# Kernel optimization log

Measured on AMD Instinct MI355X. Metric: run time of the kernel, lower is better.

## Reference

```python
import jax, jax.numpy as jnp
import numpy as np

NUM_HEADS = 12


def _attend(q, k, v, scale):
    # q: [B,H,Q,D], k/v: [B,H,K,D]
    attn = jnp.einsum('bhqd,bhkd->bhqk', q, k) * scale
    attn = jax.nn.softmax(attn, axis=-1)
    return jnp.einsum('bhqk,bhkd->bhqd', attn, v)


def setup_inputs() -> dict:
    key = jax.random.key(0)
    k1, k2, k3 = jax.random.split(key, 3)
    B, N, C = 32, 1009, 768
    x = jax.random.normal(k1, (B, N, C), dtype=jnp.float32)
    W_qkv = jax.random.normal(k2, (C, 3 * C), dtype=jnp.float32) * (C ** -0.5)
    b_qkv = jnp.zeros((3 * C,), dtype=jnp.float32)
    W_proj = jax.random.normal(k3, (C, C), dtype=jnp.float32) * (C ** -0.5)
    b_proj = jnp.zeros((C,), dtype=jnp.float32)
    return {"x": x, "W_qkv": W_qkv, "b_qkv": b_qkv, "W_proj": W_proj,
            "b_proj": b_proj, "query_len": 1, "lens_z": 432}


def reference(x, W_qkv, b_qkv, W_proj, b_proj, query_len, lens_z):
    B, N, C = x.shape
    H = NUM_HEADS
    D = C // H
    scale = D ** -0.5
    lens_x = N - query_len - lens_z

    qkv = (x @ W_qkv + b_qkv).reshape(B, N, 3, H, D)
    qkv = jnp.transpose(qkv, (2, 0, 3, 1, 4))  # [3,B,H,N,D]
    q, k, v = qkv[0], qkv[1], qkv[2]

    sl_p = slice(0, query_len)
    sl_t = slice(query_len, query_len + lens_z)
    sl_s = slice(query_len + lens_z, N)

    # prompt: local self-attention
    x_prompt = _attend(q[:, :, sl_p], k[:, :, sl_p], v[:, :, sl_p], scale)
    # template: local self-attention
    x_template = _attend(q[:, :, sl_t], k[:, :, sl_t], v[:, :, sl_t], scale)
    # search: global attention over all tokens
    x_search = _attend(q[:, :, sl_s], k, v, scale)

    def merge(y, L):
        return jnp.transpose(y, (0, 2, 1, 3)).reshape(B, L, C)

    out = jnp.concatenate([merge(x_prompt, query_len),
                           merge(x_template, lens_z),
                           merge(x_search, lens_x)], axis=1)
    return out @ W_proj + b_proj
```

## Files before the change

kernel.cpp:

```cpp
#include <hip/hip_runtime.h>

#define B_ 32
#define N_ 1009
#define C_ 768
#define H_ 12
#define D_ 64
#define M_ (B_*N_)
#define MT_ 253
#define MPAD_ (MT_*128)
#define NKV_ 1024

typedef __attribute__((ext_vector_type(4))) float f32x4;
typedef __attribute__((ext_vector_type(8))) short s16x8;

__device__ __forceinline__ unsigned short f2bf(float f) {
  union { float f; unsigned u; } x; x.f = f;
  unsigned r = x.u + 0x7fffu + ((x.u >> 16) & 1u);
  return (unsigned short)(r >> 16);
}

__device__ __forceinline__ f32x4 mfma16(s16x8 a, s16x8 b, f32x4 c) {
  return __builtin_amdgcn_mfma_f32_16x16x32_bf16(a, b, c, 0, 0, 0);
}

__device__ __forceinline__ void async16(const void* g, void* l) {
  __builtin_amdgcn_global_load_lds((const __attribute__((address_space(1))) void*)g,
                                   (__attribute__((address_space(3))) void*)l, 16, 0, 0);
}

__device__ __forceinline__ float exp2_fast(float x) {
  float r; asm("v_exp_f32 %0, %1" : "=v"(r) : "v"(x)); return r;
}

__device__ __forceinline__ unsigned cvt_pk_bf16(float lo, float hi) {
  unsigned r; asm("v_cvt_pk_bf16_f32 %0, %1, %2" : "=v"(r) : "v"(lo), "v"(hi)); return r;
}

template<int NWG>
__device__ __forceinline__ int xcd_swz(int bid) {
  constexpr int q = NWG >> 3, r = NWG & 7;
  const int x = bid & 7, l = bid >> 3;
  return (x < r ? x * (q + 1) : r * (q + 1) + (x - r) * q) + l;
}

__global__ void convert_x(const float* __restrict__ x, unsigned short* __restrict__ xb) {
  const long e = ((long)blockIdx.x * 256 + threadIdx.x) * 8;
  const long row = e / 768;
  s16x8 v;
  if (row < M_) {
#pragma unroll
    for (int j = 0; j < 8; ++j) v[j] = (short)f2bf(x[e + j]);
  } else {
    v = (s16x8){0,0,0,0,0,0,0,0};
  }
  *(s16x8*)&xb[e] = v;
}

__global__ void transpose_convert(const float* __restrict__ in, unsigned short* __restrict__ out,
                                  int R, int Ccols) {
  __shared__ float tile[64][65];
  const int tc = blockIdx.x * 64, tr = blockIdx.y * 64;
#pragma unroll
  for (int i = 0; i < 16; ++i) {
    const int e = i * 256 + threadIdx.x;
    const int r = e >> 6, c = e & 63;
    tile[r][c] = in[(long)(tr + r) * Ccols + tc + c];
  }
  __syncthreads();
#pragma unroll
  for (int i = 0; i < 16; ++i) {
    const int e = i * 256 + threadIdx.x;
    const int c = e >> 6, r = e & 63;
    out[(long)(tc + c) * R + tr + r] = f2bf(tile[r][c]);
  }
}

__global__ void zero_pad(unsigned short* __restrict__ kb, unsigned short* __restrict__ vt) {
  const int t = blockIdx.x * 256 + threadIdx.x;
  if (t >= 368640) return;
  const int d = t & 63;
  const int r = t >> 6;
  const int bh = r / 15, tok = 1009 + (r - bh * 15);
  kb[(((long)bh << 10) + tok) * 64 + d] = 0;
  const int c = t % 15, row = t / 15;
  vt[((long)row << 10) + 1009 + c] = 0;
}

template<int MODE>
__global__ __launch_bounds__(256, 4)
void gemm_bt(const unsigned short* __restrict__ A,
             const unsigned short* __restrict__ Bt,
             const float* __restrict__ bias,
             unsigned short* __restrict__ qo,
             unsigned short* __restrict__ ko,
             unsigned short* __restrict__ vo,
             float* __restrict__ fo) {
  __shared__ __align__(16) unsigned short smem[17408];
  const int tid = threadIdx.x;
  const int lane = tid & 63;
  const int wv = tid >> 6;
  constexpr int NBN = (MODE == 0) ? 18 : 6;
  const int swzid = xcd_swz<MT_ * NBN>(blockIdx.x);
  const int bm = swzid / NBN;
  const int bn = swzid - bm * NBN;
  const int row0 = bm * 128;
  const int col0 = bn * 128;
  const int wr = (wv >> 1) * 64;
  const int wc = (wv & 1) * 64;

  auto stage = [&](int bufsel, int kt) {
#pragma unroll
    for (int c = 0; c < 2; ++c) {
      const int lds_off = c * 4096 + wv * 1024;
      const int gg = c * 256 + wv * 64 + lane;
      const int row = gg >> 2;
      const int ck = ((gg & 3) ^ ((row >> 1) & 3)) << 3;
      async16(A + (long)(row0 + row) * 768 + kt + ck, (char*)smem + bufsel * 8192 + lds_off);
      async16(Bt + (long)(col0 + row) * 768 + kt + ck, (char*)smem + 16384 + bufsel * 8192 + lds_off);
    }
  };

  f32x4 acc[4][4] = {};
  stage(0, 0);
  for (int it = 0; it < 24; ++it) {
    const int buf = it & 1;
    if (it + 1 < 24) {
      stage(buf ^ 1, (it + 1) * 32);
      asm volatile("s_waitcnt vmcnt(4)" ::: "memory");
    } else {
      asm volatile("s_waitcnt vmcnt(0)" ::: "memory");
    }
    __builtin_amdgcn_s_barrier();

    const unsigned short* Asb = smem + buf * 4096;
    const unsigned short* Bsb = smem + 8192 + buf * 4096;
    s16x8 af[4], bfr[4];
#pragma unroll
    for (int m = 0; m < 4; ++m) {
      const int rA = wr + m * 16 + (lane & 15);
      af[m] = *(const s16x8*)&Asb[rA * 32 + (((lane >> 4) ^ ((rA >> 1) & 3)) << 3)];
    }
#pragma unroll
    for (int n = 0; n < 4; ++n) {
      const int rB = wc + n * 16 + (lane & 15);
      bfr[n] = *(const s16x8*)&Bsb[rB * 32 + (((lane >> 4) ^ ((rB >> 1) & 3)) << 3)];
    }
    __builtin_amdgcn_s_setprio(1);
#pragma unroll
    for (int m = 0; m < 4; ++m)
#pragma unroll
      for (int n = 0; n < 4; ++n)
        acc[m][n] = mfma16(af[m], bfr[n], acc[m][n]);
    __builtin_amdgcn_s_setprio(0);

    asm volatile("s_waitcnt lgkmcnt(0)" ::: "memory");
    __builtin_amdgcn_s_barrier();
  }

  if (MODE == 0 && col0 < 1536) {
    const int qsel = col0 < 768;
#pragma unroll
    for (int m = 0; m < 4; ++m)
#pragma unroll
      for (int j = 0; j < 4; ++j)
#pragma unroll
        for (int n = 0; n < 4; ++n) {
          const int tk = wr + m * 16 + (lane >> 4) * 4 + j;
          const int cl = wc + n * 16 + (lane & 15);
          float val = acc[m][n][j] + bias[col0 + cl];
          if (qsel) val *= 0.18033688011112042f;
          smem[tk * 136 + cl] = f2bf(val);
        }
    __syncthreads();
    unsigned short* const dst = qsel ? qo : ko;
    const int colb = col0 - (qsel ? 0 : 768);
#pragma unroll
    for (int it = 0; it < 8; ++it) {
      const int g = it * 256 + tid;
      const int tk = g >> 4;
      const int ch = (g & 15) * 8;
      const int grow = row0 + tk;
      if (grow < M_) {
        const s16x8 vv = *(const s16x8*)&smem[tk * 136 + ch];
        const int b = grow / N_;
        const int ntok = grow - b * N_;
        const int rem = colb + ch;
        const int h = rem >> 6, d = rem & 63;
        *(s16x8*)&dst[(((((long)b * H_ + h) << 10) + ntok) << 6) + d] = vv;
      }
    }
    return;
  }

  if (MODE == 0) {
#pragma unroll
    for (int m = 0; m < 4; ++m)
#pragma unroll
      for (int j = 0; j < 4; ++j)
#pragma unroll
        for (int n = 0; n < 4; ++n) {
          const int dl = wc + n * 16 + (lane & 15);
          const int tk = wr + m * 16 + (lane >> 4) * 4 + j;
          smem[dl * 136 + tk] = f2bf(acc[m][n][j] + bias[col0 + dl]);
        }
    __syncthreads();
    const int h0 = (col0 - 1536) >> 6;
    const int b0 = row0 / N_;
    const int split = (b0 + 1) * N_ - row0;
#pragma unroll
    for (int it = 0; it < 8; ++it) {
      const int g = it * 256 + tid;
      const int dl = g >> 4;
      const int t8 = (g & 15) * 8;
      const s16x8 vv = *(const s16x8*)&smem[dl * 136 + t8];
      const int hh = h0 + (dl >> 6), dd = dl & 63;
#pragma unroll
      for (int jj = 0; jj < 8; ++jj) {
        const int tkb = t8 + jj;
        const int grow = row0 + tkb;
        if (grow < M_) {
          const int bb = (tkb < split) ? b0 : b0 + 1;
          const int ntok = grow - bb * N_;
          vo[(((((long)bb * H_ + hh) << 6) + dd) << 10) + ntok] = (unsigned short)vv[jj];
        }
      }
    }
    return;
  }

#pragma unroll
  for (int m = 0; m < 4; ++m) {
#pragma unroll
    for (int j = 0; j < 4; ++j) {
      const int grow = row0 + wr + m * 16 + (lane >> 4) * 4 + j;
      if (grow < M_) {
#pragma unroll
        for (int n = 0; n < 4; ++n) {
          const int col = col0 + wc + n * 16 + (lane & 15);
          fo[(long)grow * 768 + col] = acc[m][n][j] + bias[col];
        }
      }
    }
  }
}

__global__ void misc_copy(const unsigned short* __restrict__ vt, unsigned short* __restrict__ og) {
  const int t = blockIdx.x * 256 + threadIdx.x;
  if (t >= B_ * H_ * D_) return;
  const int d = t & 63;
  const int bh = t >> 6;
  const int b = bh / H_, h = bh - b * H_;
  og[((long)b * N_) * 768 + h * 64 + d] = vt[(((long)bh << 6) + d) << 10];
}

__global__ __launch_bounds__(256, 4)
void attn_kernel(const unsigned short* __restrict__ qg,
                 const unsigned short* __restrict__ kg,
                 const unsigned short* __restrict__ vtg,
                 unsigned short* __restrict__ og) {
  __shared__ __align__(16) unsigned short Ks[2][64 * 64];
  __shared__ __align__(16) unsigned short Vts[2][64 * 64];
  __shared__ __align__(16) unsigned short Ps[64 * 64];

  const int bid = blockIdx.x;
  const int swz = (bid & 7) * 768 + (bid >> 3);
  const int tile = swz & 15;
  const int bh = swz >> 4;
  const int b = bh / H_;
  const int h = bh - b * H_;
  int qbase, qend, kstart, ktiles, kend;
  if (tile < 7) { qbase = 1 + 64 * tile;       qend = 433;  kstart = 1; ktiles = 7;  kend = 433; }
  else          { qbase = 433 + 64 * (tile-7); qend = 1009; kstart = 0; ktiles = 16; kend = 1009; }
  const long base  = (long)bh << 10;
  const long vbase = (long)bh << 6;
  const int tid = threadIdx.x, lane = tid & 63, wv = tid >> 6;
  const int q15 = lane & 15, q7 = lane & 7, g = lane >> 4;

  s16x8 qa[2];
  {
    const unsigned short* qp = qg + (base + qbase + wv * 16 + q15) * 64;
    qa[0] = *(const s16x8*)(qp + g * 8);
    qa[1] = *(const s16x8*)(qp + 32 + g * 8);
  }
  asm volatile("s_waitcnt vmcnt(0)" ::: "memory");

  f32x4 o[4] = {};
  float mrow = -1e30f, lrow = 0.f;

  auto stage = [&](int bufsel, int kb0) {
#pragma unroll
    for (int it = 0; it < 2; ++it) {
      const int ldsoff = (it * 256 + wv * 64) * 16;
      const int gr = it * 256 + wv * 64 + lane;
      const int rl = gr >> 3;
      const int cs = (gr & 7) ^ (rl & 7);
      async16(kg + ((base + kb0 + rl) << 6) + cs * 8, (char*)&Ks[bufsel][0] + ldsoff);
      async16(vtg + ((vbase + rl) << 10) + kb0 + cs * 8, (char*)&Vts[bufsel][0] + ldsoff);
    }
  };

  const int prow = wv * 16 + q15;

  stage(0, kstart);
  for (int kt = 0; kt < ktiles; ++kt) {
    const int buf = kt & 1;
    const int kbase0 = kstart + 64 * kt;
    if (kt + 1 < ktiles) {
      stage(buf ^ 1, kbase0 + 64);
      asm volatile("s_waitcnt vmcnt(4)" ::: "memory");
    } else {
      asm volatile("s_waitcnt vmcnt(0)" ::: "memory");
    }
    __builtin_amdgcn_s_barrier();

    f32x4 s4[4];
    __builtin_amdgcn_s_setprio(1);
#pragma unroll
    for (int n = 0; n < 4; ++n) {
      const int krow = n * 16 + q15;
      const int r7 = krow & 7;
      f32x4 a = {};
      a = mfma16(*(const s16x8*)&Ks[buf][krow * 64 + ((g ^ r7) << 3)],       qa[0], a);
      a = mfma16(*(const s16x8*)&Ks[buf][krow * 64 + (((4 + g) ^ r7) << 3)], qa[1], a);
      s4[n] = a;
    }
    __builtin_amdgcn_s_setprio(0);

    if (kbase0 + 64 > kend) {
#pragma unroll
      for (int n = 0; n < 4; ++n)
#pragma unroll
        for (int j = 0; j < 4; ++j)
          if (kbase0 + n * 16 + g * 4 + j >= kend) s4[n][j] = -1e30f;
    }

    float rmax = fmaxf(
        fmaxf(fmaxf(fmaxf(s4[0][0], s4[0][1]), fmaxf(s4[0][2], s4[0][3])),
              fmaxf(fmaxf(s4[1][0], s4[1][1]), fmaxf(s4[1][2], s4[1][3]))),
        fmaxf(fmaxf(fmaxf(s4[2][0], s4[2][1]), fmaxf(s4[2][2], s4[2][3])),
              fmaxf(fmaxf(s4[3][0], s4[3][1]), fmaxf(s4[3][2], s4[3][3]))));
    rmax = fmaxf(rmax, __shfl_xor(rmax, 16));
    rmax = fmaxf(rmax, __shfl_xor(rmax, 32));

    const float mnew = fmaxf(mrow, rmax);
    const float corr = exp2_fast(mrow - mnew);
    mrow = mnew;
#pragma unroll
    for (int f = 0; f < 4; ++f)
#pragma unroll
      for (int j = 0; j < 4; ++j) o[f][j] *= corr;

    float psum = 0.f;
#pragma unroll
    for (int n = 0; n < 4; ++n) {
#pragma unroll
      for (int j = 0; j < 4; ++j) {
        s4[n][j] = exp2_fast(s4[n][j] - mnew);
        psum += s4[n][j];
      }
      uint2 pw;
      pw.x = cvt_pk_bf16(s4[n][0], s4[n][1]);
      pw.y = cvt_pk_bf16(s4[n][2], s4[n][3]);
      *(uint2*)((char*)Ps + prow * 128 + (((n * 2 + (g >> 1)) ^ q7) << 4) + (g & 1) * 8) = pw;
    }
    psum += __shfl_xor(psum, 16);
    psum += __shfl_xor(psum, 32);
    lrow = lrow * corr + psum;

    s16x8 pa[2];
#pragma unroll
    for (int kf = 0; kf < 2; ++kf)
      pa[kf] = *(const s16x8*)((char*)Ps + prow * 128 + (((kf * 4 + g) ^ q7) << 4));
    __builtin_amdgcn_s_setprio(1);
#pragma unroll
    for (int f = 0; f < 4; ++f) {
      const int vrow = f * 16 + q15;
      const int v7 = vrow & 7;
#pragma unroll
      for (int kf = 0; kf < 2; ++kf) {
        const s16x8 vb = *(const s16x8*)&Vts[buf][vrow * 64 + (((kf * 4 + g) ^ v7) << 3)];
        o[f] = mfma16(vb, pa[kf], o[f]);
      }
    }
    __builtin_amdgcn_s_setprio(0);

    asm volatile("s_waitcnt lgkmcnt(0)" ::: "memory");
    __builtin_amdgcn_s_barrier();
  }

  const int qrow = qbase + wv * 16 + q15;
  if (qrow < qend) {
    const float inv = 1.0f / lrow;
    unsigned short* op = og + ((long)b * N_ + qrow) * 768 + h * 64 + g * 4;
#pragma unroll
    for (int f = 0; f < 4; ++f) {
      uint2 ow;
      ow.x = cvt_pk_bf16(o[f][0] * inv, o[f][1] * inv);
      ow.y = cvt_pk_bf16(o[f][2] * inv, o[f][3] * inv);
      *(uint2*)(op + f * 16) = ow;
    }
  }
}

extern "C" void kernel_launch(void* const* d_in, const int* in_sizes, int n_in,
                              void* d_out, int out_size, void* d_ws, size_t ws_size,
                              hipStream_t stream) {
  const float* x      = (const float*)d_in[0];
  const float* W_qkv  = (const float*)d_in[1];
  const float* b_qkv  = (const float*)d_in[2];
  const float* W_proj = (const float*)d_in[3];
  const float* b_proj = (const float*)d_in[4];
  float* out = (float*)d_out;

  unsigned short* ws = (unsigned short*)d_ws;
  unsigned short* wqkvT  = ws;
  unsigned short* wprojT = wqkvT + (long)2304 * 768;
  unsigned short* qb = wprojT + (long)768 * 768;
  const long kvsz = (long)B_ * H_ * NKV_ * D_;
  unsigned short* kb = qb + kvsz;
  unsigned short* vb = kb + kvsz;
  unsigned short* xb = vb + kvsz;
  unsigned short* attnout = xb;

  zero_pad<<<1440, 256, 0, stream>>>(kb, vb);
  convert_x<<<12144, 256, 0, stream>>>(x, xb);
  transpose_convert<<<dim3(2304 / 64, 768 / 64), 256, 0, stream>>>(W_qkv, wqkvT, 768, 2304);
  transpose_convert<<<dim3(768 / 64, 768 / 64), 256, 0, stream>>>(W_proj, wprojT, 768, 768);
  gemm_bt<0><<<MT_ * 18, 256, 0, stream>>>(xb, wqkvT, b_qkv, qb, kb, vb, nullptr);
  misc_copy<<<96, 256, 0, stream>>>(vb, attnout);
  attn_kernel<<<B_ * H_ * 16, 256, 0, stream>>>(qb, kb, vb, attnout);
  gemm_bt<1><<<MT_ * 6, 256, 0, stream>>>(attnout, wprojT, b_proj, nullptr, nullptr, nullptr, out);
}
```

Before: 405.2 us.

## Use 32x32x16 MFMA in GEMM and skip softmax rescale when max barely moves

The QKV and projection GEMM inner loop switches from 16x16x32 to 32x32x16 bf16 MFMA tiles. This changes fragment loads, the LDS swizzle pattern and the epilogue index mapping, with the goal of fewer LDS reads and instructions per FLOP. Separately, the attention kernel uses lazy rescaling: the running max, and the rescale of the output and row sum, are only updated when some row's new max exceeds the old one by more than 8 in log2 units. This saves the correction multiplies but lets unnormalised exponentials grow up to 2^8, which carries some risk of bf16 precision loss in P.

```diff
diff --git a/kernel.cpp b/kernel.cpp
--- a/kernel.cpp
+++ b/kernel.cpp
@@ -11,6 +11,7 @@
 #define NKV_ 1024
 
 typedef __attribute__((ext_vector_type(4))) float f32x4;
+typedef __attribute__((ext_vector_type(16))) float f32x16;
 typedef __attribute__((ext_vector_type(8))) short s16x8;
 
 __device__ __forceinline__ unsigned short f2bf(float f) {
@@ -21,6 +22,10 @@
 
 __device__ __forceinline__ f32x4 mfma16(s16x8 a, s16x8 b, f32x4 c) {
   return __builtin_amdgcn_mfma_f32_16x16x32_bf16(a, b, c, 0, 0, 0);
+}
+
+__device__ __forceinline__ f32x16 mfma32(s16x8 a, s16x8 b, f32x16 c) {
+  return __builtin_amdgcn_mfma_f32_32x32x16_bf16(a, b, c, 0, 0, 0);
 }
 
 __device__ __forceinline__ void async16(const void* g, void* l) {
@@ -107,6 +112,7 @@
   const int col0 = bn * 128;
   const int wr = (wv >> 1) * 64;
   const int wc = (wv & 1) * 64;
+  const int l31 = lane & 31, hi = lane >> 5;
 
   auto stage = [&](int bufsel, int kt) {
 #pragma unroll
@@ -114,13 +120,13 @@
       const int lds_off = c * 4096 + wv * 1024;
       const int gg = c * 256 + wv * 64 + lane;
       const int row = gg >> 2;
-      const int ck = ((gg & 3) ^ ((row >> 1) & 3)) << 3;
+      const int ck = ((gg & 3) ^ (((row >> 1) ^ (row >> 3)) & 3)) << 3;
       async16(A + (long)(row0 + row) * 768 + kt + ck, (char*)smem + bufsel * 8192 + lds_off);
       async16(Bt + (long)(col0 + row) * 768 + kt + ck, (char*)smem + 16384 + bufsel * 8192 + lds_off);
     }
   };
 
-  f32x4 acc[4][4] = {};
+  f32x16 acc[2][2] = {};
   stage(0, 0);
   for (int it = 0; it < 24; ++it) {
     const int buf = it & 1;
@@ -134,23 +140,27 @@
 
     const unsigned short* Asb = smem + buf * 4096;
     const unsigned short* Bsb = smem + 8192 + buf * 4096;
-    s16x8 af[4], bfr[4];
-#pragma unroll
-    for (int m = 0; m < 4; ++m) {
-      const int rA = wr + m * 16 + (lane & 15);
-      af[m] = *(const s16x8*)&Asb[rA * 32 + (((lane >> 4) ^ ((rA >> 1) & 3)) << 3)];
-    }
-#pragma unroll
-    for (int n = 0; n < 4; ++n) {
-      const int rB = wc + n * 16 + (lane & 15);
-      bfr[n] = *(const s16x8*)&Bsb[rB * 32 + (((lane >> 4) ^ ((rB >> 1) & 3)) << 3)];
+    s16x8 af[2][2], bfr[2][2];
+#pragma unroll
+    for (int b2 = 0; b2 < 2; ++b2) {
+      const int rA = wr + b2 * 32 + l31;
+      const int swA = ((rA >> 1) ^ (rA >> 3)) & 3;
+      const int rB = wc + b2 * 32 + l31;
+      const int swB = ((rB >> 1) ^ (rB >> 3)) & 3;
+#pragma unroll
+      for (int kin = 0; kin < 2; ++kin) {
+        af[b2][kin]  = *(const s16x8*)&Asb[rA * 32 + (((kin * 2 + hi) ^ swA) << 3)];
+        bfr[b2][kin] = *(const s16x8*)&Bsb[rB * 32 + (((kin * 2 + hi) ^ swB) << 3)];
+      }
     }
     __builtin_amdgcn_s_setprio(1);
 #pragma unroll
-    for (int m = 0; m < 4; ++m)
-#pragma unroll
-      for (int n = 0; n < 4; ++n)
-        acc[m][n] = mfma16(af[m], bfr[n], acc[m][n]);
+    for (int kin = 0; kin < 2; ++kin)
+#pragma unroll
+      for (int m2 = 0; m2 < 2; ++m2)
+#pragma unroll
+        for (int n2 = 0; n2 < 2; ++n2)
+          acc[m2][n2] = mfma32(af[m2][kin], bfr[n2][kin], acc[m2][n2]);
     __builtin_amdgcn_s_setprio(0);
 
     asm volatile("s_waitcnt lgkmcnt(0)" ::: "memory");
@@ -160,14 +170,14 @@
   if (MODE == 0 && col0 < 1536) {
     const int qsel = col0 < 768;
 #pragma unroll
-    for (int m = 0; m < 4; ++m)
-#pragma unroll
-      for (int j = 0; j < 4; ++j)
-#pragma unroll
-        for (int n = 0; n < 4; ++n) {
-          const int tk = wr + m * 16 + (lane >> 4) * 4 + j;
-          const int cl = wc + n * 16 + (lane & 15);
-          float val = acc[m][n][j] + bias[col0 + cl];
+    for (int m2 = 0; m2 < 2; ++m2)
+#pragma unroll
+      for (int n2 = 0; n2 < 2; ++n2)
+#pragma unroll
+        for (int r = 0; r < 16; ++r) {
+          const int tk = wr + m2 * 32 + (r & 3) + ((r >> 2) << 3) + (hi << 2);
+          const int cl = wc + n2 * 32 + l31;
+          float val = acc[m2][n2][r] + bias[col0 + cl];
           if (qsel) val *= 0.18033688011112042f;
           smem[tk * 136 + cl] = f2bf(val);
         }
@@ -194,14 +204,14 @@
 
   if (MODE == 0) {
 #pragma unroll
-    for (int m = 0; m < 4; ++m)
-#pragma unroll
-      for (int j = 0; j < 4; ++j)
-#pragma unroll
-        for (int n = 0; n < 4; ++n) {
-          const int dl = wc + n * 16 + (lane & 15);
-          const int tk = wr + m * 16 + (lane >> 4) * 4 + j;
-          smem[dl * 136 + tk] = f2bf(acc[m][n][j] + bias[col0 + dl]);
+    for (int m2 = 0; m2 < 2; ++m2)
+#pragma unroll
+      for (int n2 = 0; n2 < 2; ++n2)
+#pragma unroll
+        for (int r = 0; r < 16; ++r) {
+          const int dl = wc + n2 * 32 + l31;
+          const int tk = wr + m2 * 32 + (r & 3) + ((r >> 2) << 3) + (hi << 2);
+          smem[dl * 136 + tk] = f2bf(acc[m2][n2][r] + bias[col0 + dl]);
         }
     __syncthreads();
     const int h0 = (col0 - 1536) >> 6;
@@ -229,15 +239,15 @@
   }
 
 #pragma unroll
-  for (int m = 0; m < 4; ++m) {
-#pragma unroll
-    for (int j = 0; j < 4; ++j) {
-      const int grow = row0 + wr + m * 16 + (lane >> 4) * 4 + j;
+  for (int m2 = 0; m2 < 2; ++m2) {
+#pragma unroll
+    for (int r = 0; r < 16; ++r) {
+      const int grow = row0 + wr + m2 * 32 + (r & 3) + ((r >> 2) << 3) + (hi << 2);
       if (grow < M_) {
 #pragma unroll
-        for (int n = 0; n < 4; ++n) {
-          const int col = col0 + wc + n * 16 + (lane & 15);
-          fo[(long)grow * 768 + col] = acc[m][n][j] + bias[col];
+        for (int n2 = 0; n2 < 2; ++n2) {
+          const int col = col0 + wc + n2 * 32 + l31;
+          fo[(long)grow * 768 + col] = acc[m2][n2][r] + bias[col];
         }
       }
     }
@@ -342,13 +352,17 @@
     rmax = fmaxf(rmax, __shfl_xor(rmax, 16));
     rmax = fmaxf(rmax, __shfl_xor(rmax, 32));
 
-    const float mnew = fmaxf(mrow, rmax);
-    const float corr = exp2_fast(mrow - mnew);
-    mrow = mnew;
-#pragma unroll
-    for (int f = 0; f < 4; ++f)
-#pragma unroll
-      for (int j = 0; j < 4; ++j) o[f][j] *= corr;
+    if (!__all(rmax <= mrow + 8.f)) {
+      const float mnew = fmaxf(mrow, rmax);
+      const float corr = exp2_fast(mrow - mnew);
+      mrow = mnew;
+      lrow *= corr;
+#pragma unroll
+      for (int f = 0; f < 4; ++f)
+#pragma unroll
+        for (int j = 0; j < 4; ++j) o[f][j] *= corr;
+    }
+    const float mnew = mrow;
 
     float psum = 0.f;
 #pragma unroll
@@ -365,7 +379,7 @@
     }
     psum += __shfl_xor(psum, 16);
     psum += __shfl_xor(psum, 32);
-    lrow = lrow * corr + psum;
+    lrow += psum;
 
     s16x8 pa[2];
 #pragma unroll
```

New measurement: 415.5 us. +2.6%, slower.
